# Kernel tuning notes

Measured on AMD Instinct MI355X. Metric: run time of the kernel, lower is better.

Reference implementation:

```python
import jax, jax.numpy as jnp
import numpy as np
from jax import lax

B, H, W, C, G, K = 2, 64, 64, 256, 8, 9
CQ = C // 4  # PConv partial channels
HC = C // G  # head channels
PTS = np.array([[-1, -1], [-1, 0], [-1, 1], [0, -1], [0, 0], [0, 1],
                [1, -1], [1, 0], [1, 1]], np.float32)  # (K,2) as (dx,dy)


def setup_inputs() -> dict:
    key = jax.random.key(0)
    ks = jax.random.split(key, 13)
    n = lambda i, shp, s: jax.random.normal(ks[i], shp, jnp.float32) * s
    return {
        'x': jax.random.normal(ks[0], (B, H, W, C), jnp.float32),
        'qkv_w': n(1, (C, 3 * C), C ** -0.5),
        'qkv_b': n(2, (3 * C,), 0.02),
        'dw_w': n(3, (3, 3, 1, 3 * C), 1.0 / 3.0),
        'dw_b': n(4, (3 * C,), 0.02),
        'off_pconv_w': n(5, (G, CQ, CQ, 3, 3), (CQ * 9) ** -0.5),
        'off_w': n(6, (G, 2 * K, C), 0.1 * C ** -0.5),
        'off_b': n(7, (G, 2 * K), 0.1),
        'mask_pconv_w': n(8, (CQ, CQ, 3, 3), (CQ * 9) ** -0.5),
        'mask_w': n(9, (K, C), C ** -0.5),
        'mask_b': n(10, (K,), 0.02),
        'proj_w': n(11, (C, C), C ** -0.5),
        'proj_b': n(12, (C,), 0.02),
    }


def _dwconv_nhwc(x, w, b):
    # depthwise 3x3, pad 1, stride 1; x (B,H,W,ch), w (3,3,1,ch)
    ch = x.shape[-1]
    y = lax.conv_general_dilated(x, w, (1, 1), 'SAME',
                                 dimension_numbers=('NHWC', 'HWIO', 'NHWC'),
                                 feature_group_count=ch)
    return y + b


def _pconv_nchw(x, w):
    # partial conv: 3x3 (no bias) on first CQ channels, rest untouched
    dc = w.shape[0]
    x1 = lax.conv_general_dilated(x[:, :dc], w, (1, 1), 'SAME',
                                  dimension_numbers=('NCHW', 'OIHW', 'NCHW'))
    return jnp.concatenate([x1, x[:, dc:]], axis=1)


def _flow_warp(x, flow):
    # x (N,Cc,Hh,Ww), flow (N,2K,Hh,Ww) -> (N,Cc,K,Hh,Ww)
    # bilinear grid_sample, border padding, align_corners=True == sampling at
    # absolute pixel coords with coordinate clamping.
    N, Cc, Hh, Ww = x.shape
    Kk = flow.shape[1] // 2
    fl = flow.reshape(N, Kk, 2, Hh, Ww).transpose(0, 3, 4, 1, 2)  # (N,H,W,K,2)
    gy, gx = jnp.meshgrid(jnp.arange(Hh, dtype=x.dtype),
                          jnp.arange(Ww, dtype=x.dtype), indexing='ij')
    base = jnp.stack([gx, gy], axis=-1)  # (H,W,2) in (x,y) order
    coords = base[None, :, :, None, :] + fl  # (N,H,W,K,2)
    cx = jnp.clip(coords[..., 0], 0.0, Ww - 1)
    cy = jnp.clip(coords[..., 1], 0.0, Hh - 1)
    x0 = jnp.floor(cx)
    y0 = jnp.floor(cy)
    wx = (cx - x0).reshape(N, 1, -1)
    wy = (cy - y0).reshape(N, 1, -1)
    x0i = x0.astype(jnp.int32)
    y0i = y0.astype(jnp.int32)
    x1i = jnp.minimum(x0i + 1, Ww - 1)
    y1i = jnp.minimum(y0i + 1, Hh - 1)
    xf = x.reshape(N, Cc, Hh * Ww)

    def gather(yi, xi):
        idx = (yi * Ww + xi).reshape(N, -1)  # (N, H*W*K)
        return jax.vmap(lambda im, ix: im[:, ix])(xf, idx)  # (N,Cc,H*W*K)

    v00 = gather(y0i, x0i)
    v01 = gather(y0i, x1i)
    v10 = gather(y1i, x0i)
    v11 = gather(y1i, x1i)
    out = (v00 * (1 - wx) * (1 - wy) + v01 * wx * (1 - wy)
           + v10 * (1 - wx) * wy + v11 * wx * wy)
    return out.reshape(N, Cc, Hh, Ww, Kk).transpose(0, 1, 4, 2, 3)


def reference(x, qkv_w, qkv_b, dw_w, dw_b, off_pconv_w, off_w, off_b,
              mask_pconv_w, mask_w, mask_b, proj_w, proj_b):
    Bb, Hh, Ww, Cc = x.shape
    P = Hh * Ww
    scale = HC ** -0.5
    # qkv projection + depthwise conv (NHWC)
    qkv = x @ qkv_w + qkv_b                       # (B,H,W,3C)
    qkv = _dwconv_nhwc(qkv, dw_w, dw_b)
    q = qkv[..., :Cc]                             # (B,H,W,C)
    k_map = jnp.transpose(qkv[..., Cc:2 * Cc], (0, 3, 1, 2))   # (B,C,H,W)
    v_map = jnp.transpose(qkv[..., 2 * Cc:], (0, 3, 1, 2))     # (B,C,H,W)
    q_nchw = jnp.transpose(q, (0, 3, 1, 2))

    # shared mask conv: PConv + 1x1 -> (B,K,H,W)
    xm = _pconv_nchw(q_nchw, mask_pconv_w)
    mask = jnp.einsum('bchw,oc->bohw', xm, mask_w) + mask_b[None, :, None, None]

    # base offsets per group: points_pool * (2g+1), flattened (dx,dy) pairs
    base = jnp.asarray(np.stack([(PTS * (2 * g + 1)).reshape(-1)
                                 for g in range(G)], axis=0))  # (G,2K)

    k_list, v_list = [], []
    for g in range(G):
        xo = _pconv_nchw(q_nchw, off_pconv_w[g])
        off = (jnp.einsum('bchw,oc->bohw', xo, off_w[g])
               + off_b[g][None, :, None, None]
               + base[g][None, :, None, None])  # (B,2K,H,W)
        sl = slice(g * HC, (g + 1) * HC)
        k_list.append(_flow_warp(k_map[:, sl], off) * mask[:, None])
        v_list.append(_flow_warp(v_map[:, sl], off) * mask[:, None])

    # stack (G,B,hc,K,H,W) -> (B,G,P,K,hc)
    def arrange(lst):
        t = jnp.stack(lst, axis=0).transpose(1, 0, 4, 5, 3, 2)
        return t.reshape(Bb, G, P, K, HC)

    k = arrange(k_list)
    v = arrange(v_list)
    qh = (q.reshape(Bb, Hh, Ww, G, HC).transpose(0, 3, 1, 2, 4)
          .reshape(Bb, G, P, HC)) * scale

    attn = jnp.einsum('bgpc,bgpkc->bgpk', qh, k)
    attn = jax.nn.softmax(attn, axis=-1)
    out = jnp.einsum('bgpk,bgpkc->bgpc', attn, v)       # (B,G,P,hc)
    out = out.transpose(0, 2, 1, 3).reshape(Bb, Hh, Ww, Cc)
    return out @ proj_w + proj_b
```

## Files before the change

### kernel.cpp

```cpp
#include <hip/hip_runtime.h>

typedef unsigned short u16;
typedef short bf16x8 __attribute__((ext_vector_type(8)));
typedef float f32x4 __attribute__((ext_vector_type(4)));

#define PP 4096
#define KPT 9

__device__ __forceinline__ u16 f2b(float f) {
    union { float f; unsigned int u; } v; v.f = f;
    unsigned int u = v.u;
    unsigned int r = u + 0x7FFFu + ((u >> 16) & 1u);
    return (u16)(r >> 16);
}
__device__ __forceinline__ float b2f(u16 b) {
    union { unsigned int u; float f; } v; v.u = ((unsigned int)b) << 16;
    return v.f;
}

__global__ __launch_bounds__(256) void convert_inputs(
        const float* __restrict__ x, const float* __restrict__ qkv_w,
        const float* __restrict__ proj_w,
        u16* __restrict__ x_b, u16* __restrict__ qkv_wT_b, u16* __restrict__ proj_wT_b) {
    int idx = blockIdx.x * 256 + threadIdx.x;
    if (idx < 2097152) { x_b[idx] = f2b(x[idx]); return; }
    int i2 = idx - 2097152;
    if (i2 < 196608) {
        int r = i2 / 768, c = i2 % 768;
        qkv_wT_b[c * 256 + r] = f2b(qkv_w[i2]);
        return;
    }
    int i3 = i2 - 196608;
    int r = i3 >> 8, c = i3 & 255;
    proj_wT_b[c * 256 + r] = f2b(proj_w[i3]);
}

template<bool OUT_BF16>
__global__ __launch_bounds__(256) void mfma_gemm(
        const u16* __restrict__ A, const u16* __restrict__ BT,
        const float* __restrict__ bias, void* __restrict__ out,
        int M, int N, int K) {
    __shared__ u16 As[128][40];
    __shared__ u16 Bs[64][40];
    int tid = threadIdx.x;
    int row0 = blockIdx.x * 128, col0 = blockIdx.y * 64;
    int wid = tid >> 6, lane = tid & 63;
    int wr = wid >> 1, wc = wid & 1;
    int l15 = lane & 15, lhi = lane >> 4;
    f32x4 acc[4][2] = {};
    for (int k0 = 0; k0 < K; k0 += 32) {
        #pragma unroll
        for (int q = 0; q < 2; q++) {
            int idx = tid + q * 256;
            int r = idx >> 2, kc = (idx & 3) * 8;
            *(bf16x8*)&As[r][kc] = *(const bf16x8*)&A[(size_t)(row0 + r) * K + k0 + kc];
        }
        {
            int r = tid >> 2, kc = (tid & 3) * 8;
            *(bf16x8*)&Bs[r][kc] = *(const bf16x8*)&BT[(size_t)(col0 + r) * K + k0 + kc];
        }
        __syncthreads();
        bf16x8 bfr[2];
        #pragma unroll
        for (int j = 0; j < 2; j++)
            bfr[j] = *(const bf16x8*)&Bs[wc * 32 + j * 16 + l15][lhi * 8];
        #pragma unroll
        for (int i = 0; i < 4; i++) {
            bf16x8 afr = *(const bf16x8*)&As[wr * 64 + i * 16 + l15][lhi * 8];
            #pragma unroll
            for (int j = 0; j < 2; j++)
                acc[i][j] = __builtin_amdgcn_mfma_f32_16x16x32_bf16(afr, bfr[j], acc[i][j], 0, 0, 0);
        }
        __syncthreads();
    }
    #pragma unroll
    for (int i = 0; i < 4; i++) {
        int row = row0 + wr * 64 + i * 16 + lhi * 4;
        #pragma unroll
        for (int j = 0; j < 2; j++) {
            int col = col0 + wc * 32 + j * 16 + l15;
            float bv = bias[col];
            #pragma unroll
            for (int r = 0; r < 4; r++) {
                float v = acc[i][j][r] + bv;
                if (OUT_BF16) ((u16*)out)[(size_t)(row + r) * N + col] = f2b(v);
                else          ((float*)out)[(size_t)(row + r) * N + col] = v;
            }
        }
    }
}

__global__ __launch_bounds__(256) void dwconv_b(const u16* __restrict__ qkv_b,
        const float* __restrict__ dww, const float* __restrict__ dwb,
        u16* __restrict__ out) {
    int idx = blockIdx.x * 256 + threadIdx.x;
    int c8 = (idx % 96) * 8;
    int pix = idx / 96;
    int w = pix & 63, h = (pix >> 6) & 63, b = pix >> 12;
    float acc[8];
    #pragma unroll
    for (int j = 0; j < 8; j++) acc[j] = dwb[c8 + j];
    #pragma unroll
    for (int ky = 0; ky < 3; ky++) {
        int hh = h + ky - 1;
        if (hh < 0 || hh >= 64) continue;
        #pragma unroll
        for (int kx = 0; kx < 3; kx++) {
            int ww = w + kx - 1;
            if (ww < 0 || ww >= 64) continue;
            bf16x8 v = *(const bf16x8*)&qkv_b[((size_t)((b * 64 + hh) * 64 + ww)) * 768 + c8];
            #pragma unroll
            for (int j = 0; j < 8; j++)
                acc[j] += b2f((u16)v[j]) * dww[(ky * 3 + kx) * 768 + c8 + j];
        }
    }
    bf16x8 o;
    #pragma unroll
    for (int j = 0; j < 8; j++) o[j] = (short)f2b(acc[j]);
    *(bf16x8*)&out[(size_t)idx * 8] = o;
}

__global__ void make_cw(const float* __restrict__ off_pconv_w,
        const float* __restrict__ off_w, const float* __restrict__ off_b,
        const float* __restrict__ mask_pconv_w, const float* __restrict__ mask_w,
        const float* __restrict__ mask_b, u16* __restrict__ cwT_b,
        float* __restrict__ cb) {
    int k = blockIdx.x;
    int o = threadIdx.x;
    float val = 0.f;
    if (o < 153) {
        if (k < 576) {
            int patch = k >> 6, i = k & 63;
            if (o < 144) {
                int g = o / 18, oo = o % 18;
                for (int c = 0; c < 64; c++)
                    val += off_w[(g * 18 + oo) * 256 + c] *
                           off_pconv_w[((g * 64 + c) * 64 + i) * 9 + patch];
            } else {
                int oo = o - 144;
                for (int c = 0; c < 64; c++)
                    val += mask_w[oo * 256 + c] * mask_pconv_w[(c * 64 + i) * 9 + patch];
            }
        } else {
            int j = k - 576;
            if (o < 144) {
                int g = o / 18, oo = o % 18;
                val = off_w[(g * 18 + oo) * 256 + 64 + j];
            } else {
                val = mask_w[(o - 144) * 256 + 64 + j];
            }
        }
    }
    cwT_b[o * 768 + k] = f2b(val);
    if (k == 0) {
        float bv = 0.f;
        if (o < 144) {
            int g = o / 18, oo = o % 18;
            const float PTSf[18] = {-1,-1,-1,0,-1,1,0,-1,0,0,0,1,1,-1,1,0,1,1};
            bv = off_b[g * 18 + oo] + PTSf[oo] * (float)(2 * g + 1);
        } else if (o < 153) {
            bv = mask_b[o - 144];
        }
        cb[o] = bv;
    }
}

__global__ __launch_bounds__(256) void offmask_mfma(const u16* __restrict__ qdw_b,
        const u16* __restrict__ cwT_b, const float* __restrict__ cb,
        float* __restrict__ offmask) {
    __shared__ u16 As[32][40];
    __shared__ u16 Bs[160][40];
    int tid = threadIdx.x;
    int p0 = blockIdx.x * 32;
    int wid = tid >> 6, lane = tid & 63;
    int wr = wid >> 1, wc = wid & 1;
    int l15 = lane & 15, lhi = lane >> 4;
    f32x4 acc[5] = {};
    for (int k0 = 0; k0 < 768; k0 += 32) {
        if (tid < 128) {
            int r = tid >> 2, kc = (tid & 3) * 8;
            int pixel = p0 + r;
            int w = pixel & 63, h = (pixel >> 6) & 63, b = pixel >> 12;
            bf16x8 v = {};
            if (k0 < 576) {
                int patch = k0 >> 6;
                int dy = patch / 3 - 1, dx = patch % 3 - 1;
                int hh = h + dy, ww = w + dx;
                if (hh >= 0 && hh < 64 && ww >= 0 && ww < 64)
                    v = *(const bf16x8*)&qdw_b[((size_t)((b * 64 + hh) * 64 + ww)) * 768 + (k0 & 63) + kc];
            } else {
                v = *(const bf16x8*)&qdw_b[((size_t)((b * 64 + h) * 64 + w)) * 768 + 64 + (k0 - 576) + kc];
            }
            *(bf16x8*)&As[r][kc] = v;
        }
        for (int idx = tid; idx < 640; idx += 256) {
            int r = idx >> 2, kc = (idx & 3) * 8;
            *(bf16x8*)&Bs[r][kc] = *(const bf16x8*)&cwT_b[r * 768 + k0 + kc];
        }
        __syncthreads();
        bf16x8 afr = *(const bf16x8*)&As[wr * 16 + l15][lhi * 8];
        #pragma unroll
        for (int j = 0; j < 5; j++) {
            bf16x8 bfr = *(const bf16x8*)&Bs[wc * 80 + j * 16 + l15][lhi * 8];
            acc[j] = __builtin_amdgcn_mfma_f32_16x16x32_bf16(afr, bfr, acc[j], 0, 0, 0);
        }
        __syncthreads();
    }
    int row = p0 + wr * 16 + lhi * 4;
    #pragma unroll
    for (int j = 0; j < 5; j++) {
        int col = wc * 80 + j * 16 + l15;
        float bv = cb[col];
        #pragma unroll
        for (int r = 0; r < 4; r++)
            offmask[(size_t)(row + r) * 160 + col] = acc[j][r] + bv;
    }
}

__global__ __launch_bounds__(256) void deform_attn(const u16* __restrict__ qdw_b,
        const float* __restrict__ offmask, u16* __restrict__ attn_b) {
    int tid = threadIdx.x;
    int unit = blockIdx.x * 8 + (tid >> 5);
    int lane = tid & 31;
    int b = unit / (8 * PP);
    int rem = unit % (8 * PP);
    int g = rem / PP;
    int p = rem % PP;
    int w = p & 63, h = p >> 6;
    const float scale = 0.17677669529663687f;
    float qv = b2f(qdw_b[((size_t)((b * 64 + h) * 64 + w)) * 768 + g * 32 + lane]) * scale;
    const float* om = offmask + (size_t)(b * PP + p) * 160;
    float logit[KPT], vs[KPT];
    #pragma unroll
    for (int k_ = 0; k_ < KPT; k_++) {
        float dx = om[g * 18 + 2 * k_];
        float dy = om[g * 18 + 2 * k_ + 1];
        float cx = fminf(fmaxf((float)w + dx, 0.f), 63.f);
        float cy = fminf(fmaxf((float)h + dy, 0.f), 63.f);
        float x0f = floorf(cx), y0f = floorf(cy);
        float wx = cx - x0f, wy = cy - y0f;
        int x0 = (int)x0f, y0 = (int)y0f;
        int x1 = min(x0 + 1, 63), y1 = min(y0 + 1, 63);
        int ch_k = 256 + g * 32 + lane;
        int ch_v = 512 + g * 32 + lane;
        size_t b00 = ((size_t)((b * 64 + y0) * 64 + x0)) * 768;
        size_t b01 = ((size_t)((b * 64 + y0) * 64 + x1)) * 768;
        size_t b10 = ((size_t)((b * 64 + y1) * 64 + x0)) * 768;
        size_t b11 = ((size_t)((b * 64 + y1) * 64 + x1)) * 768;
        float w00 = (1.f - wx) * (1.f - wy), w01 = wx * (1.f - wy);
        float w10 = (1.f - wx) * wy,         w11 = wx * wy;
        float kk = b2f(qdw_b[b00 + ch_k]) * w00 + b2f(qdw_b[b01 + ch_k]) * w01
                 + b2f(qdw_b[b10 + ch_k]) * w10 + b2f(qdw_b[b11 + ch_k]) * w11;
        float vv = b2f(qdw_b[b00 + ch_v]) * w00 + b2f(qdw_b[b01 + ch_v]) * w01
                 + b2f(qdw_b[b10 + ch_v]) * w10 + b2f(qdw_b[b11 + ch_v]) * w11;
        float m = om[144 + k_];
        float part = qv * kk;
        part += __shfl_xor(part, 16);
        part += __shfl_xor(part, 8);
        part += __shfl_xor(part, 4);
        part += __shfl_xor(part, 2);
        part += __shfl_xor(part, 1);
        logit[k_] = part * m;
        vs[k_] = vv * m;
    }
    float mx = logit[0];
    #pragma unroll
    for (int k_ = 1; k_ < KPT; k_++) mx = fmaxf(mx, logit[k_]);
    float s = 0.f, e[KPT];
    #pragma unroll
    for (int k_ = 0; k_ < KPT; k_++) { e[k_] = expf(logit[k_] - mx); s += e[k_]; }
    float inv = 1.f / s;
    float outv = 0.f;
    #pragma unroll
    for (int k_ = 0; k_ < KPT; k_++) outv += e[k_] * vs[k_];
    attn_b[(size_t)(b * PP + p) * 256 + g * 32 + lane] = f2b(outv * inv);
}

extern "C" void kernel_launch(void* const* d_in, const int* in_sizes, int n_in,
                              void* d_out, int out_size, void* d_ws, size_t ws_size,
                              hipStream_t stream) {
    const float* x            = (const float*)d_in[0];
    const float* qkv_w        = (const float*)d_in[1];
    const float* qkv_b        = (const float*)d_in[2];
    const float* dw_w         = (const float*)d_in[3];
    const float* dw_b         = (const float*)d_in[4];
    const float* off_pconv_w  = (const float*)d_in[5];
    const float* off_w        = (const float*)d_in[6];
    const float* off_b        = (const float*)d_in[7];
    const float* mask_pconv_w = (const float*)d_in[8];
    const float* mask_w       = (const float*)d_in[9];
    const float* mask_b       = (const float*)d_in[10];
    const float* proj_w       = (const float*)d_in[11];
    const float* proj_b       = (const float*)d_in[12];

    char* ws = (char*)d_ws;
    u16*   x_b        = (u16*)(ws);                       size_t off = 8192ull*256*2;
    u16*   qkv_wT_b   = (u16*)(ws + off);                 off += 768ull*256*2;
    u16*   proj_wT_b  = (u16*)(ws + off);                 off += 256ull*256*2;
    u16*   qkv_bf     = (u16*)(ws + off);                 off += 8192ull*768*2;
    u16*   qdw_b      = (u16*)(ws + off);                 off += 8192ull*768*2;
    u16*   cwT_b      = (u16*)(ws + off);                 off += 160ull*768*2;
    float* cb         = (float*)(ws + off);               off += 256*4;
    float* offmask    = (float*)(ws + off);               off += 8192ull*160*4;
    u16*   attn_b     = (u16*)(ws + off);                 off += 8192ull*256*2;

    convert_inputs<<<9216, 256, 0, stream>>>(x, qkv_w, proj_w, x_b, qkv_wT_b, proj_wT_b);
    make_cw<<<768, 160, 0, stream>>>(off_pconv_w, off_w, off_b,
                                     mask_pconv_w, mask_w, mask_b, cwT_b, cb);
    mfma_gemm<true><<<dim3(64, 12), 256, 0, stream>>>(x_b, qkv_wT_b, qkv_b,
                                                      qkv_bf, 8192, 768, 256);
    dwconv_b<<<3072, 256, 0, stream>>>(qkv_bf, dw_w, dw_b, qdw_b);
    offmask_mfma<<<256, 256, 0, stream>>>(qdw_b, cwT_b, cb, offmask);
    deform_attn<<<8192, 256, 0, stream>>>(qdw_b, offmask, attn_b);
    mfma_gemm<false><<<dim3(64, 4), 256, 0, stream>>>(attn_b, proj_wT_b, proj_b,
                                                      d_out, 8192, 256, 256);
}
```

Measured before the change: 199.0 us.

## Precompute bilinear sample points and vectorize deform attention to two channels per lane

Adds a kernel that precomputes, per pixel/group/point, a packed base index, edge flags, fractional weights and mask as a float4, so the attention kernel no longer recomputes coordinates redundantly across 32 lanes. The attention kernel now processes two bf16 channels per lane with 32-bit loads, halving the threads per (pixel, group) and the shuffle steps. This trades an extra launch and a ~9MB intermediate buffer round-trip for fewer, wider gathers and less per-lane ALU work.

Measured after the change: 193.7 us. 2.6% less time.

```diff
diff --git a/kernel.cpp b/kernel.cpp
--- a/kernel.cpp
+++ b/kernel.cpp
@@ -1,6 +1,7 @@
 #include <hip/hip_runtime.h>
 
 typedef unsigned short u16;
+typedef unsigned int u32;
 typedef short bf16x8 __attribute__((ext_vector_type(8)));
 typedef float f32x4 __attribute__((ext_vector_type(4)));
 
@@ -217,63 +218,98 @@
     }
 }
 
+__global__ __launch_bounds__(256) void precompute_pts(const float* __restrict__ offmask,
+        float4* __restrict__ pre) {
+    int idx = blockIdx.x * 256 + threadIdx.x;
+    if (idx >= 2 * PP * 72) return;
+    int item = idx % 72;
+    int pix = idx / 72;
+    int g = item / 9, k = item % 9;
+    int w = pix & 63, h = (pix >> 6) & 63;
+    const float* om = offmask + (size_t)pix * 160;
+    float dx = om[g * 18 + 2 * k];
+    float dy = om[g * 18 + 2 * k + 1];
+    float m  = om[144 + k];
+    float cx = fminf(fmaxf((float)w + dx, 0.f), 63.f);
+    float cy = fminf(fmaxf((float)h + dy, 0.f), 63.f);
+    float x0f = floorf(cx), y0f = floorf(cy);
+    int x0 = (int)x0f, y0 = (int)y0f;
+    u32 idx00 = (u32)((pix & ~4095) | (y0 << 6) | x0);
+    u32 pk = idx00 | ((x0 < 63) ? 0x10000u : 0u) | ((y0 < 63) ? 0x20000u : 0u);
+    float4 o;
+    o.x = __uint_as_float(pk);
+    o.y = cx - x0f;
+    o.z = cy - y0f;
+    o.w = m;
+    pre[idx] = o;
+}
+
 __global__ __launch_bounds__(256) void deform_attn(const u16* __restrict__ qdw_b,
-        const float* __restrict__ offmask, u16* __restrict__ attn_b) {
+        const float4* __restrict__ pre, u16* __restrict__ attn_b) {
     int tid = threadIdx.x;
-    int unit = blockIdx.x * 8 + (tid >> 5);
-    int lane = tid & 31;
-    int b = unit / (8 * PP);
-    int rem = unit % (8 * PP);
-    int g = rem / PP;
-    int p = rem % PP;
-    int w = p & 63, h = p >> 6;
+    int unit = blockIdx.x * 16 + (tid >> 4);
+    int cl = tid & 15;
+    int b = unit >> 15;
+    int g = (unit >> 12) & 7;
+    int p = unit & 4095;
+    int pix = (b << 12) | p;
     const float scale = 0.17677669529663687f;
-    float qv = b2f(qdw_b[((size_t)((b * 64 + h) * 64 + w)) * 768 + g * 32 + lane]) * scale;
-    const float* om = offmask + (size_t)(b * PP + p) * 160;
-    float logit[KPT], vs[KPT];
+    u32 qu = *(const u32*)&qdw_b[(size_t)pix * 768 + g * 32 + 2 * cl];
+    float qlo = __uint_as_float(qu << 16) * scale;
+    float qhi = __uint_as_float(qu & 0xFFFF0000u) * scale;
+    const float4* pp = pre + (size_t)pix * 72 + g * 9;
+    const char* base = (const char*)qdw_b;
+    u32 ckb = (u32)(512 + (g * 32 + 2 * cl) * 2);
+    float logit[KPT], vlo[KPT], vhi[KPT];
     #pragma unroll
     for (int k_ = 0; k_ < KPT; k_++) {
-        float dx = om[g * 18 + 2 * k_];
-        float dy = om[g * 18 + 2 * k_ + 1];
-        float cx = fminf(fmaxf((float)w + dx, 0.f), 63.f);
-        float cy = fminf(fmaxf((float)h + dy, 0.f), 63.f);
-        float x0f = floorf(cx), y0f = floorf(cy);
-        float wx = cx - x0f, wy = cy - y0f;
-        int x0 = (int)x0f, y0 = (int)y0f;
-        int x1 = min(x0 + 1, 63), y1 = min(y0 + 1, 63);
-        int ch_k = 256 + g * 32 + lane;
-        int ch_v = 512 + g * 32 + lane;
-        size_t b00 = ((size_t)((b * 64 + y0) * 64 + x0)) * 768;
-        size_t b01 = ((size_t)((b * 64 + y0) * 64 + x1)) * 768;
-        size_t b10 = ((size_t)((b * 64 + y1) * 64 + x0)) * 768;
-        size_t b11 = ((size_t)((b * 64 + y1) * 64 + x1)) * 768;
+        float4 q4 = pp[k_];
+        u32 pk = __float_as_uint(q4.x);
+        float wx = q4.y, wy = q4.z, m = q4.w;
+        u32 o00 = (pk & 0xFFFFu) * 1536u + ckb;
+        u32 dX = (pk & 0x10000u) ? 1536u : 0u;
+        u32 dY = (pk & 0x20000u) ? 98304u : 0u;
+        u32 o01 = o00 + dX, o10 = o00 + dY, o11 = o00 + dY + dX;
+        u32 k00 = *(const u32*)(base + o00);
+        u32 v00 = *(const u32*)(base + o00 + 512);
+        u32 k01 = *(const u32*)(base + o01);
+        u32 v01 = *(const u32*)(base + o01 + 512);
+        u32 k10 = *(const u32*)(base + o10);
+        u32 v10 = *(const u32*)(base + o10 + 512);
+        u32 k11 = *(const u32*)(base + o11);
+        u32 v11 = *(const u32*)(base + o11 + 512);
         float w00 = (1.f - wx) * (1.f - wy), w01 = wx * (1.f - wy);
         float w10 = (1.f - wx) * wy,         w11 = wx * wy;
-        float kk = b2f(qdw_b[b00 + ch_k]) * w00 + b2f(qdw_b[b01 + ch_k]) * w01
-                 + b2f(qdw_b[b10 + ch_k]) * w10 + b2f(qdw_b[b11 + ch_k]) * w11;
-        float vv = b2f(qdw_b[b00 + ch_v]) * w00 + b2f(qdw_b[b01 + ch_v]) * w01
-                 + b2f(qdw_b[b10 + ch_v]) * w10 + b2f(qdw_b[b11 + ch_v]) * w11;
-        float m = om[144 + k_];
-        float part = qv * kk;
-        part += __shfl_xor(part, 16);
+        float klo = __uint_as_float(k00 << 16) * w00 + __uint_as_float(k01 << 16) * w01
+                  + __uint_as_float(k10 << 16) * w10 + __uint_as_float(k11 << 16) * w11;
+        float khi = __uint_as_float(k00 & 0xFFFF0000u) * w00 + __uint_as_float(k01 & 0xFFFF0000u) * w01
+                  + __uint_as_float(k10 & 0xFFFF0000u) * w10 + __uint_as_float(k11 & 0xFFFF0000u) * w11;
+        float Vlo = __uint_as_float(v00 << 16) * w00 + __uint_as_float(v01 << 16) * w01
+                  + __uint_as_float(v10 << 16) * w10 + __uint_as_float(v11 << 16) * w11;
+        float Vhi = __uint_as_float(v00 & 0xFFFF0000u) * w00 + __uint_as_float(v01 & 0xFFFF0000u) * w01
+                  + __uint_as_float(v10 & 0xFFFF0000u) * w10 + __uint_as_float(v11 & 0xFFFF0000u) * w11;
+        float part = qlo * klo + qhi * khi;
         part += __shfl_xor(part, 8);
         part += __shfl_xor(part, 4);
         part += __shfl_xor(part, 2);
         part += __shfl_xor(part, 1);
         logit[k_] = part * m;
-        vs[k_] = vv * m;
+        vlo[k_] = Vlo * m;
+        vhi[k_] = Vhi * m;
     }
     float mx = logit[0];
     #pragma unroll
     for (int k_ = 1; k_ < KPT; k_++) mx = fmaxf(mx, logit[k_]);
-    float s = 0.f, e[KPT];
-    #pragma unroll
-    for (int k_ = 0; k_ < KPT; k_++) { e[k_] = expf(logit[k_] - mx); s += e[k_]; }
+    float s = 0.f;
+    #pragma unroll
+    for (int k_ = 0; k_ < KPT; k_++) { logit[k_] = expf(logit[k_] - mx); s += logit[k_]; }
     float inv = 1.f / s;
-    float outv = 0.f;
-    #pragma unroll
-    for (int k_ = 0; k_ < KPT; k_++) outv += e[k_] * vs[k_];
-    attn_b[(size_t)(b * PP + p) * 256 + g * 32 + lane] = f2b(outv * inv);
+    float olo = 0.f, ohi = 0.f;
+    #pragma unroll
+    for (int k_ = 0; k_ < KPT; k_++) { olo += logit[k_] * vlo[k_]; ohi += logit[k_] * vhi[k_]; }
+    olo *= inv; ohi *= inv;
+    u32 outw = (u32)f2b(olo) | ((u32)f2b(ohi) << 16);
+    *(u32*)&attn_b[(size_t)pix * 256 + g * 32 + 2 * cl] = outw;
 }
 
 extern "C" void kernel_launch(void* const* d_in, const int* in_sizes, int n_in,
@@ -303,6 +339,7 @@
     float* cb         = (float*)(ws + off);               off += 256*4;
     float* offmask    = (float*)(ws + off);               off += 8192ull*160*4;
     u16*   attn_b     = (u16*)(ws + off);                 off += 8192ull*256*2;
+    float4* pre       = (float4*)(ws + off);              off += 589824ull*16;
 
     convert_inputs<<<9216, 256, 0, stream>>>(x, qkv_w, proj_w, x_b, qkv_wT_b, proj_wT_b);
     make_cw<<<768, 160, 0, stream>>>(off_pconv_w, off_w, off_b,
@@ -311,7 +348,8 @@
                                                       qkv_bf, 8192, 768, 256);
     dwconv_b<<<3072, 256, 0, stream>>>(qkv_bf, dw_w, dw_b, qdw_b);
     offmask_mfma<<<256, 256, 0, stream>>>(qdw_b, cwT_b, cb, offmask);
-    deform_attn<<<8192, 256, 0, stream>>>(qdw_b, offmask, attn_b);
+    precompute_pts<<<2304, 256, 0, stream>>>(offmask, pre);
+    deform_attn<<<4096, 256, 0, stream>>>(qdw_b, pre, attn_b);
     mfma_gemm<false><<<dim3(64, 4), 256, 0, stream>>>(attn_b, proj_wT_b, proj_b,
                                                       d_out, 8192, 256, 256);
 }
```
